# Kernel optimization log

Hardware: AMD Instinct MI355X
Metric: run time of the kernel (lower is better)

## Reference

```python
import jax, jax.numpy as jnp
import numpy as np

N = 8192
NHID = 256

def setup_inputs() -> dict:
    key = jax.random.key(0)
    k1, k2, k3 = jax.random.split(key, 3)
    x = jax.random.normal(k1, (N, NHID), dtype=jnp.float32)
    # dense (row-normalized-ish) adjacency; values in [0,1)
    adj = jax.random.uniform(k2, (N, N), dtype=jnp.float32) / N
    W = jax.random.normal(k3, (NHID, NHID), dtype=jnp.float32) * (1.0 / np.sqrt(NHID))
    b = jnp.zeros((NHID,), dtype=jnp.float32)
    return {"x": x, "adj": adj, "W": W, "b": b}

def reference(x, adj, W, b):
    # GCN layer: adj @ (x W) + b, then ReLU (dropout is identity at inference)
    support = x @ W + b            # [N, nhid]
    h = adj @ support              # [N, nhid]  (sparse-style aggregation, dense here)
    h = jax.nn.relu(h)
    # outer-product structure reconstruction
    return h @ h.T                 # [N, N]
```

## Files before the change

kernel.cpp:

```cpp
#include <hip/hip_runtime.h>
#include <hip/hip_bf16.h>
#include <stdint.h>

#define GLOBAL_AS __attribute__((address_space(1)))
#define LDS_AS    __attribute__((address_space(3)))

typedef __attribute__((ext_vector_type(8))) short          short8;
typedef __attribute__((ext_vector_type(4))) float          floatx4;
typedef __attribute__((ext_vector_type(4))) unsigned short ushort4v;

static __device__ __forceinline__ unsigned short f2bf_bits(float f) {
    union { float f; unsigned int u; } v; v.f = f;
    unsigned int r = v.u + 0x7FFFu + ((v.u >> 16) & 1u);
    return (unsigned short)(r >> 16);
}

static __device__ __forceinline__ floatx4 mfma16(short8 a, short8 b, floatx4 c) {
    return __builtin_amdgcn_mfma_f32_16x16x32_bf16(a, b, c, 0, 0, 0);
}

template<int BM, int BN, int BK, int WM, int WN, bool A_F32, bool B_F32, int EPI>
__global__ __launch_bounds__(256, 2)
void gemm_bt(const void* __restrict__ Ap, const void* __restrict__ Bp,
             const float* __restrict__ bias, void* __restrict__ Cp,
             int lda, int ldb, int ldc, int klen, long pstride)
{
    constexpr int NWM = BM / WM;
    constexpr int NWN = BN / WN;
    static_assert(NWM * NWN == 4, "4 waves per block");
    constexpr int FM = WM / 16;
    constexpr int FN = WN / 16;

    __shared__ __align__(16) unsigned short As[BM * BK];
    __shared__ __align__(16) unsigned short Bs[BN * BK];

    const int tid  = threadIdx.x;
    const int lane = tid & 63;
    const int wave = tid >> 6;
    const int wm   = (wave % NWM) * WM;
    const int wn   = (wave / NWM) * WN;
    const int quad = lane >> 4;
    const int l16  = lane & 15;
    const long m0 = (long)blockIdx.x * BM;
    const long n0 = (long)blockIdx.y * BN;
    const long k0 = (long)blockIdx.z * (long)klen;

    floatx4 acc[FM][FN];
#pragma unroll
    for (int i = 0; i < FM; ++i)
#pragma unroll
        for (int j = 0; j < FN; ++j) {
            floatx4 z = {0.f, 0.f, 0.f, 0.f};
            acc[i][j] = z;
        }

    for (int kk = 0; kk < klen; kk += BK) {
        {
            constexpr int CH = BM * BK / 8;
            if constexpr (A_F32) {
                const float* A = (const float*)Ap;
#pragma unroll
                for (int c0 = 0; c0 < CH; c0 += 256) {
                    int c   = c0 + tid;
                    int row = c / (BK / 8);
                    int col = (c % (BK / 8)) * 8;
                    const float* src = A + (m0 + row) * (long)lda + (k0 + kk + col);
                    floatx4 f0 = *(const floatx4*)(src);
                    floatx4 f1 = *(const floatx4*)(src + 4);
                    union { unsigned short u[8]; short8 v; } pk;
                    pk.u[0] = f2bf_bits(f0.x); pk.u[1] = f2bf_bits(f0.y);
                    pk.u[2] = f2bf_bits(f0.z); pk.u[3] = f2bf_bits(f0.w);
                    pk.u[4] = f2bf_bits(f1.x); pk.u[5] = f2bf_bits(f1.y);
                    pk.u[6] = f2bf_bits(f1.z); pk.u[7] = f2bf_bits(f1.w);
                    *(short8*)&As[c * 8] = pk.v;
                }
            } else {
                const unsigned short* A = (const unsigned short*)Ap;
#pragma unroll
                for (int c0 = 0; c0 < CH; c0 += 256) {
                    int c   = c0 + tid;
                    int row = c / (BK / 8);
                    int col = (c % (BK / 8)) * 8;
                    const unsigned short* src = A + (m0 + row) * (long)lda + (k0 + kk + col);
                    __builtin_amdgcn_global_load_lds((const GLOBAL_AS unsigned int*)src,
                                                     (LDS_AS unsigned int*)&As[c * 8],
                                                     16, 0, 0);
                }
            }
        }
        {
            constexpr int CH = BN * BK / 8;
            if constexpr (B_F32) {
                const float* B = (const float*)Bp;
#pragma unroll
                for (int c0 = 0; c0 < CH; c0 += 256) {
                    int c   = c0 + tid;
                    int row = c / (BK / 8);
                    int col = (c % (BK / 8)) * 8;
                    const float* src = B + (n0 + row) * (long)ldb + (k0 + kk + col);
                    floatx4 f0 = *(const floatx4*)(src);
                    floatx4 f1 = *(const floatx4*)(src + 4);
                    union { unsigned short u[8]; short8 v; } pk;
                    pk.u[0] = f2bf_bits(f0.x); pk.u[1] = f2bf_bits(f0.y);
                    pk.u[2] = f2bf_bits(f0.z); pk.u[3] = f2bf_bits(f0.w);
                    pk.u[4] = f2bf_bits(f1.x); pk.u[5] = f2bf_bits(f1.y);
                    pk.u[6] = f2bf_bits(f1.z); pk.u[7] = f2bf_bits(f1.w);
                    *(short8*)&Bs[c * 8] = pk.v;
                }
            } else {
                const unsigned short* B = (const unsigned short*)Bp;
#pragma unroll
                for (int c0 = 0; c0 < CH; c0 += 256) {
                    int c   = c0 + tid;
                    int row = c / (BK / 8);
                    int col = (c % (BK / 8)) * 8;
                    const unsigned short* src = B + (n0 + row) * (long)ldb + (k0 + kk + col);
                    __builtin_amdgcn_global_load_lds((const GLOBAL_AS unsigned int*)src,
                                                     (LDS_AS unsigned int*)&Bs[c * 8],
                                                     16, 0, 0);
                }
            }
        }
        __syncthreads();

#pragma unroll
        for (int ks = 0; ks < BK; ks += 32) {
            short8 af[FM], bfr[FN];
#pragma unroll
            for (int i = 0; i < FM; ++i)
                af[i] = *(const short8*)&As[(wm + i * 16 + l16) * BK + ks + quad * 8];
#pragma unroll
            for (int j = 0; j < FN; ++j)
                bfr[j] = *(const short8*)&Bs[(wn + j * 16 + l16) * BK + ks + quad * 8];
#pragma unroll
            for (int i = 0; i < FM; ++i)
#pragma unroll
                for (int j = 0; j < FN; ++j)
                    acc[i][j] = mfma16(af[i], bfr[j], acc[i][j]);
        }
        __syncthreads();
    }

#pragma unroll
    for (int i = 0; i < FM; ++i)
#pragma unroll
        for (int j = 0; j < FN; ++j)
#pragma unroll
            for (int v = 0; v < 4; ++v) {
                long r = m0 + wm + i * 16 + quad * 4 + v;
                long c = n0 + wn + j * 16 + l16;
                float val = acc[i][j][v];
                if constexpr (EPI == 0) {
                    val += bias[r];
                    ((unsigned short*)Cp)[r * (long)ldc + c] = f2bf_bits(val);
                } else if constexpr (EPI == 2) {
                    ((float*)Cp)[r * (long)ldc + c] = val;
                } else {
                    ((float*)Cp)[(long)blockIdx.z * pstride + r * (long)ldc + c] = val;
                }
            }
}

__global__ void transpose_w_kernel(const float* __restrict__ W, unsigned short* __restrict__ Wt)
{
    int idx = blockIdx.x * 256 + threadIdx.x;
    int n = idx >> 8;
    int k = idx & 255;
    Wt[n * 256 + k] = f2bf_bits(W[k * 256 + n]);
}

__global__ void reduce_relu_kernel(const float* __restrict__ p0, const float* __restrict__ p1,
                                   unsigned short* __restrict__ h)
{
    int i = (blockIdx.x * 256 + threadIdx.x) * 4;
    floatx4 a = *(const floatx4*)(p0 + i);
    floatx4 b = *(const floatx4*)(p1 + i);
    ushort4v o;
    o.x = f2bf_bits(fmaxf(a.x + b.x, 0.f));
    o.y = f2bf_bits(fmaxf(a.y + b.y, 0.f));
    o.z = f2bf_bits(fmaxf(a.z + b.z, 0.f));
    o.w = f2bf_bits(fmaxf(a.w + b.w, 0.f));
    *(ushort4v*)&h[i] = o;
}

extern "C" void kernel_launch(void* const* d_in, const int* in_sizes, int n_in,
                              void* d_out, int out_size, void* d_ws, size_t ws_size,
                              hipStream_t stream)
{
    const float* x   = (const float*)d_in[0];
    const float* adj = (const float*)d_in[1];
    const float* W   = (const float*)d_in[2];
    const float* b   = (const float*)d_in[3];
    float* out = (float*)d_out;

    char* ws = (char*)d_ws;
    unsigned short* Wt   = (unsigned short*)(ws);
    unsigned short* supT = (unsigned short*)(ws + 131072);
    unsigned short* h    = (unsigned short*)(ws + 4325376);
    float*          parts= (float*)         (ws + 8519680);
    const long PSTRIDE = 8192L * 256L;

    transpose_w_kernel<<<256, 256, 0, stream>>>(W, Wt);

    gemm_bt<32, 256, 64, 32, 64, false, true, 0>
        <<<dim3(8, 32, 1), 256, 0, stream>>>(Wt, x, b, supT, 256, 256, 8192, 256, 0);

    gemm_bt<32, 256, 64, 32, 64, true, false, 3>
        <<<dim3(256, 1, 2), 256, 0, stream>>>(adj, supT, nullptr, parts,
                                              8192, 8192, 256, 4096, PSTRIDE);

    reduce_relu_kernel<<<2048, 256, 0, stream>>>(parts, parts + PSTRIDE, h);

    gemm_bt<128, 128, 64, 64, 64, false, false, 2>
        <<<dim3(64, 64, 1), 256, 0, stream>>>(h, h, nullptr, out, 256, 256, 8192, 256, 0);
}
```

Before: 558.5 us.

## Specialize aggregation with split-K prefetch and LDS-free symmetric HH^T kernel

Replaces the generic adj@support GEMM with a dedicated kernel using 64-row tiles, 4-way split-K and register prefetch of the next fp32 adj tile to overlap global loads with MFMA work. The reduce kernel now sums four partials. The final h·hᵀ GEMM becomes a kernel that loads MFMA fragments directly from global memory without LDS and writes transposed vectorized float4 stores, relying on output symmetry. This trades more partial-sum traffic and cache-dependent operand reuse for better latency hiding and coalesced output writes.

```diff
diff --git a/kernel.cpp b/kernel.cpp
--- a/kernel.cpp
+++ b/kernel.cpp
@@ -23,7 +23,7 @@
 __global__ __launch_bounds__(256, 2)
 void gemm_bt(const void* __restrict__ Ap, const void* __restrict__ Bp,
              const float* __restrict__ bias, void* __restrict__ Cp,
-             int lda, int ldb, int ldc, int klen, long pstride)
+             int lda, int ldb, int ldc, int klen)
 {
     constexpr int NWM = BM / WM;
     constexpr int NWN = BN / WN;
@@ -43,7 +43,6 @@
     const int l16  = lane & 15;
     const long m0 = (long)blockIdx.x * BM;
     const long n0 = (long)blockIdx.y * BN;
-    const long k0 = (long)blockIdx.z * (long)klen;
 
     floatx4 acc[FM][FN];
 #pragma unroll
@@ -61,10 +60,8 @@
                 const float* A = (const float*)Ap;
 #pragma unroll
                 for (int c0 = 0; c0 < CH; c0 += 256) {
-                    int c   = c0 + tid;
-                    int row = c / (BK / 8);
-                    int col = (c % (BK / 8)) * 8;
-                    const float* src = A + (m0 + row) * (long)lda + (k0 + kk + col);
+                    int c = c0 + tid, row = c / (BK / 8), col = (c % (BK / 8)) * 8;
+                    const float* src = A + (m0 + row) * (long)lda + (kk + col);
                     floatx4 f0 = *(const floatx4*)(src);
                     floatx4 f1 = *(const floatx4*)(src + 4);
                     union { unsigned short u[8]; short8 v; } pk;
@@ -78,13 +75,10 @@
                 const unsigned short* A = (const unsigned short*)Ap;
 #pragma unroll
                 for (int c0 = 0; c0 < CH; c0 += 256) {
-                    int c   = c0 + tid;
-                    int row = c / (BK / 8);
-                    int col = (c % (BK / 8)) * 8;
-                    const unsigned short* src = A + (m0 + row) * (long)lda + (k0 + kk + col);
+                    int c = c0 + tid, row = c / (BK / 8), col = (c % (BK / 8)) * 8;
+                    const unsigned short* src = A + (m0 + row) * (long)lda + (kk + col);
                     __builtin_amdgcn_global_load_lds((const GLOBAL_AS unsigned int*)src,
-                                                     (LDS_AS unsigned int*)&As[c * 8],
-                                                     16, 0, 0);
+                                                     (LDS_AS unsigned int*)&As[c * 8], 16, 0, 0);
                 }
             }
         }
@@ -94,10 +88,8 @@
                 const float* B = (const float*)Bp;
 #pragma unroll
                 for (int c0 = 0; c0 < CH; c0 += 256) {
-                    int c   = c0 + tid;
-                    int row = c / (BK / 8);
-                    int col = (c % (BK / 8)) * 8;
-                    const float* src = B + (n0 + row) * (long)ldb + (k0 + kk + col);
+                    int c = c0 + tid, row = c / (BK / 8), col = (c % (BK / 8)) * 8;
+                    const float* src = B + (n0 + row) * (long)ldb + (kk + col);
                     floatx4 f0 = *(const floatx4*)(src);
                     floatx4 f1 = *(const floatx4*)(src + 4);
                     union { unsigned short u[8]; short8 v; } pk;
@@ -111,13 +103,10 @@
                 const unsigned short* B = (const unsigned short*)Bp;
 #pragma unroll
                 for (int c0 = 0; c0 < CH; c0 += 256) {
-                    int c   = c0 + tid;
-                    int row = c / (BK / 8);
-                    int col = (c % (BK / 8)) * 8;
-                    const unsigned short* src = B + (n0 + row) * (long)ldb + (k0 + kk + col);
+                    int c = c0 + tid, row = c / (BK / 8), col = (c % (BK / 8)) * 8;
+                    const unsigned short* src = B + (n0 + row) * (long)ldb + (kk + col);
                     __builtin_amdgcn_global_load_lds((const GLOBAL_AS unsigned int*)src,
-                                                     (LDS_AS unsigned int*)&Bs[c * 8],
-                                                     16, 0, 0);
+                                                     (LDS_AS unsigned int*)&Bs[c * 8], 16, 0, 0);
                 }
             }
         }
@@ -149,16 +138,161 @@
             for (int v = 0; v < 4; ++v) {
                 long r = m0 + wm + i * 16 + quad * 4 + v;
                 long c = n0 + wn + j * 16 + l16;
-                float val = acc[i][j][v];
-                if constexpr (EPI == 0) {
-                    val += bias[r];
-                    ((unsigned short*)Cp)[r * (long)ldc + c] = f2bf_bits(val);
-                } else if constexpr (EPI == 2) {
-                    ((float*)Cp)[r * (long)ldc + c] = val;
-                } else {
-                    ((float*)Cp)[(long)blockIdx.z * pstride + r * (long)ldc + c] = val;
-                }
+                float val = acc[i][j][v] + bias[r];
+                ((unsigned short*)Cp)[r * (long)ldc + c] = f2bf_bits(val);
             }
+}
+
+__global__ __launch_bounds__(256, 2)
+void agg_kernel(const float* __restrict__ adj, const unsigned short* __restrict__ supT,
+                float* __restrict__ parts)
+{
+    constexpr int BK = 64, KLEN = 2048;
+    constexpr long PST = 8192L * 256L;
+
+    __shared__ __align__(16) unsigned short As[64 * BK];
+    __shared__ __align__(16) unsigned short Bs[256 * BK];
+
+    const int tid  = threadIdx.x;
+    const int lane = tid & 63;
+    const int wave = tid >> 6;
+    const int wm   = (wave & 1) * 32;
+    const int wn   = (wave >> 1) * 128;
+    const int quad = lane >> 4;
+    const int l16  = lane & 15;
+    const long m0 = (long)blockIdx.x * 64;
+    const long k0 = (long)blockIdx.z * (long)KLEN;
+
+    const int ar = tid >> 3;
+    const int ac = (tid & 7) * 8;
+    const float* aptr0 = adj + (m0 + ar) * 8192L + k0 + ac;
+    const float* aptr1 = aptr0 + 32 * 8192L;
+
+    floatx4 acc[2][8];
+#pragma unroll
+    for (int i = 0; i < 2; ++i)
+#pragma unroll
+        for (int j = 0; j < 8; ++j) {
+            floatx4 z = {0.f, 0.f, 0.f, 0.f};
+            acc[i][j] = z;
+        }
+
+    floatx4 a0 = *(const floatx4*)(aptr0);
+    floatx4 a1 = *(const floatx4*)(aptr0 + 4);
+    floatx4 a2 = *(const floatx4*)(aptr1);
+    floatx4 a3 = *(const floatx4*)(aptr1 + 4);
+
+    for (int kk = 0; kk < KLEN; kk += BK) {
+#pragma unroll
+        for (int c0 = 0; c0 < 2048; c0 += 256) {
+            int c = c0 + tid, row = c >> 3, col = (c & 7) * 8;
+            const unsigned short* src = supT + row * 8192L + (k0 + kk + col);
+            __builtin_amdgcn_global_load_lds((const GLOBAL_AS unsigned int*)src,
+                                             (LDS_AS unsigned int*)&Bs[c * 8], 16, 0, 0);
+        }
+        {
+            union { unsigned short u[8]; short8 v; } p0, p1;
+            p0.u[0] = f2bf_bits(a0.x); p0.u[1] = f2bf_bits(a0.y);
+            p0.u[2] = f2bf_bits(a0.z); p0.u[3] = f2bf_bits(a0.w);
+            p0.u[4] = f2bf_bits(a1.x); p0.u[5] = f2bf_bits(a1.y);
+            p0.u[6] = f2bf_bits(a1.z); p0.u[7] = f2bf_bits(a1.w);
+            p1.u[0] = f2bf_bits(a2.x); p1.u[1] = f2bf_bits(a2.y);
+            p1.u[2] = f2bf_bits(a2.z); p1.u[3] = f2bf_bits(a2.w);
+            p1.u[4] = f2bf_bits(a3.x); p1.u[5] = f2bf_bits(a3.y);
+            p1.u[6] = f2bf_bits(a3.z); p1.u[7] = f2bf_bits(a3.w);
+            *(short8*)&As[tid * 8] = p0.v;
+            *(short8*)&As[(tid + 256) * 8] = p1.v;
+        }
+        __syncthreads();
+
+        if (kk + BK < KLEN) {
+            aptr0 += BK; aptr1 += BK;
+            a0 = *(const floatx4*)(aptr0);
+            a1 = *(const floatx4*)(aptr0 + 4);
+            a2 = *(const floatx4*)(aptr1);
+            a3 = *(const floatx4*)(aptr1 + 4);
+        }
+
+#pragma unroll
+        for (int ks = 0; ks < BK; ks += 32) {
+            short8 af[2], bfr[8];
+#pragma unroll
+            for (int i = 0; i < 2; ++i)
+                af[i] = *(const short8*)&As[(wm + i * 16 + l16) * BK + ks + quad * 8];
+#pragma unroll
+            for (int j = 0; j < 8; ++j)
+                bfr[j] = *(const short8*)&Bs[(wn + j * 16 + l16) * BK + ks + quad * 8];
+#pragma unroll
+            for (int i = 0; i < 2; ++i)
+#pragma unroll
+                for (int j = 0; j < 8; ++j)
+                    acc[i][j] = mfma16(af[i], bfr[j], acc[i][j]);
+        }
+        __syncthreads();
+    }
+
+    float* dst = parts + (long)blockIdx.z * PST;
+#pragma unroll
+    for (int i = 0; i < 2; ++i)
+#pragma unroll
+        for (int j = 0; j < 8; ++j)
+#pragma unroll
+            for (int v = 0; v < 4; ++v) {
+                long r = m0 + wm + i * 16 + quad * 4 + v;
+                long c = wn + j * 16 + l16;
+                dst[r * 256L + c] = acc[i][j][v];
+            }
+}
+
+__global__ __launch_bounds__(256, 2)
+void hht_kernel(const unsigned short* __restrict__ h, float* __restrict__ out)
+{
+    const int tid  = threadIdx.x;
+    const int lane = tid & 63;
+    const int wave = tid >> 6;
+    const int wm   = (wave & 1) * 64;
+    const int wn   = (wave >> 1) * 64;
+    const int quad = lane >> 4;
+    const int l16  = lane & 15;
+    const long m0 = (long)blockIdx.x * 128;
+    const long n0 = (long)blockIdx.y * 128;
+
+    floatx4 acc[4][4];
+#pragma unroll
+    for (int i = 0; i < 4; ++i)
+#pragma unroll
+        for (int j = 0; j < 4; ++j) {
+            floatx4 z = {0.f, 0.f, 0.f, 0.f};
+            acc[i][j] = z;
+        }
+
+    const unsigned short* arow = h + (m0 + wm + l16) * 256L + quad * 8;
+    const unsigned short* brow = h + (n0 + wn + l16) * 256L + quad * 8;
+
+#pragma unroll
+    for (int ks = 0; ks < 256; ks += 32) {
+        short8 af[4], bfr[4];
+#pragma unroll
+        for (int i = 0; i < 4; ++i)
+            af[i] = *(const short8*)(arow + i * 16 * 256L + ks);
+#pragma unroll
+        for (int j = 0; j < 4; ++j)
+            bfr[j] = *(const short8*)(brow + j * 16 * 256L + ks);
+#pragma unroll
+        for (int i = 0; i < 4; ++i)
+#pragma unroll
+            for (int j = 0; j < 4; ++j)
+                acc[i][j] = mfma16(af[i], bfr[j], acc[i][j]);
+    }
+
+#pragma unroll
+    for (int i = 0; i < 4; ++i)
+#pragma unroll
+        for (int j = 0; j < 4; ++j) {
+            long rt = n0 + wn + j * 16 + l16;
+            long ct = m0 + wm + i * 16 + quad * 4;
+            *(floatx4*)&out[rt * 8192L + ct] = acc[i][j];
+        }
 }
 
 __global__ void transpose_w_kernel(const float* __restrict__ W, unsigned short* __restrict__ Wt)
@@ -169,17 +303,19 @@
     Wt[n * 256 + k] = f2bf_bits(W[k * 256 + n]);
 }
 
-__global__ void reduce_relu_kernel(const float* __restrict__ p0, const float* __restrict__ p1,
-                                   unsigned short* __restrict__ h)
-{
+__global__ void reduce_relu_kernel(const float* __restrict__ p, unsigned short* __restrict__ h)
+{
+    constexpr long PST = 8192L * 256L;
     int i = (blockIdx.x * 256 + threadIdx.x) * 4;
-    floatx4 a = *(const floatx4*)(p0 + i);
-    floatx4 b = *(const floatx4*)(p1 + i);
+    floatx4 a = *(const floatx4*)(p + i);
+    floatx4 b = *(const floatx4*)(p + PST + i);
+    floatx4 c = *(const floatx4*)(p + 2 * PST + i);
+    floatx4 d = *(const floatx4*)(p + 3 * PST + i);
     ushort4v o;
-    o.x = f2bf_bits(fmaxf(a.x + b.x, 0.f));
-    o.y = f2bf_bits(fmaxf(a.y + b.y, 0.f));
-    o.z = f2bf_bits(fmaxf(a.z + b.z, 0.f));
-    o.w = f2bf_bits(fmaxf(a.w + b.w, 0.f));
+    o.x = f2bf_bits(fmaxf(a.x + b.x + c.x + d.x, 0.f));
+    o.y = f2bf_bits(fmaxf(a.y + b.y + c.y + d.y, 0.f));
+    o.z = f2bf_bits(fmaxf(a.z + b.z + c.z + d.z, 0.f));
+    o.w = f2bf_bits(fmaxf(a.w + b.w + c.w + d.w, 0.f));
     *(ushort4v*)&h[i] = o;
 }
 
@@ -194,23 +330,19 @@
     float* out = (float*)d_out;
 
     char* ws = (char*)d_ws;
-    unsigned short* Wt   = (unsigned short*)(ws);
-    unsigned short* supT = (unsigned short*)(ws + 131072);
-    unsigned short* h    = (unsigned short*)(ws + 4325376);
-    float*          parts= (float*)         (ws + 8519680);
-    const long PSTRIDE = 8192L * 256L;
+    unsigned short* Wt    = (unsigned short*)(ws);
+    unsigned short* supT  = (unsigned short*)(ws + 131072);
+    unsigned short* h     = (unsigned short*)(ws + 4325376);
+    float*          parts = (float*)         (ws + 8519680);
 
     transpose_w_kernel<<<256, 256, 0, stream>>>(W, Wt);
 
     gemm_bt<32, 256, 64, 32, 64, false, true, 0>
-        <<<dim3(8, 32, 1), 256, 0, stream>>>(Wt, x, b, supT, 256, 256, 8192, 256, 0);
-
-    gemm_bt<32, 256, 64, 32, 64, true, false, 3>
-        <<<dim3(256, 1, 2), 256, 0, stream>>>(adj, supT, nullptr, parts,
-                                              8192, 8192, 256, 4096, PSTRIDE);
-
-    reduce_relu_kernel<<<2048, 256, 0, stream>>>(parts, parts + PSTRIDE, h);
-
-    gemm_bt<128, 128, 64, 64, 64, false, false, 2>
-        <<<dim3(64, 64, 1), 256, 0, stream>>>(h, h, nullptr, out, 256, 256, 8192, 256, 0);
-}
+        <<<dim3(8, 32, 1), 256, 0, stream>>>(Wt, x, b, supT, 256, 256, 8192, 256);
+
+    agg_kernel<<<dim3(128, 1, 4), 256, 0, stream>>>(adj, supT, parts);
+
+    reduce_relu_kernel<<<2048, 256, 0, stream>>>(parts, h);
+
+    hht_kernel<<<dim3(64, 64, 1), 256, 0, stream>>>(h, out);
+}
```

Measured after the change: 629.2 us. 12.7% more time.
